# Optimization experiments

Measured on AMD Instinct MI355X. Metric: run time of the kernel, lower is better.

The kernel has to match this reference:

```python
import jax, jax.numpy as jnp
import numpy as np

N_NODES = 100000
EPS = 1e-5


def _layernorm(x, g, b):
    # per-node layer norm over feature dim
    mu = jnp.mean(x, axis=-1, keepdims=True)
    var = jnp.mean(jnp.square(x - mu), axis=-1, keepdims=True)
    return (x - mu) * jax.lax.rsqrt(var + EPS) * g + b


def _gcn_conv(x, W, b, src, dst, n_nodes):
    # GCNConv: xW, then symmetric-normalized aggregation with self-loops.
    xw = x @ W  # [N, out]
    ones = jnp.ones(src.shape[0], dtype=x.dtype)
    deg = jax.ops.segment_sum(ones, dst, num_segments=n_nodes) + 1.0  # +1 self loop
    dinv = jax.lax.rsqrt(deg)  # [N]
    norm = dinv[src] * dinv[dst]  # [E]
    msg = xw[src] * norm[:, None]  # [E, out]  <- dominant memory traffic
    agg = jax.ops.segment_sum(msg, dst, num_segments=n_nodes)
    agg = agg + xw * (dinv * dinv)[:, None]  # self-loop contribution
    return agg + b


def setup_inputs() -> dict:
    key = jax.random.key(0)
    ks = jax.random.split(key, 16)
    in_c, hid, out_c = 128, 64, 32
    E = 1_600_000
    d = {}
    d['x'] = jax.random.normal(ks[0], (N_NODES, in_c), dtype=jnp.float32)
    d['edge_index'] = jax.random.randint(ks[1], (2, E), 0, N_NODES, dtype=jnp.int64)

    def lin(k, fi, fo):
        s = 1.0 / np.sqrt(fi)
        k1, k2 = jax.random.split(k)
        return (jax.random.uniform(k1, (fi, fo), jnp.float32, -s, s),
                jax.random.uniform(k2, (fo,), jnp.float32, -s, s))

    d['W1'], d['b1'] = lin(ks[2], in_c, hid)
    d['g1'], d['be1'] = jnp.ones((hid,), jnp.float32), jnp.zeros((hid,), jnp.float32)
    d['W2'], d['b2'] = lin(ks[3], hid, 2 * hid)
    d['g2'], d['be2'] = jnp.ones((2 * hid,), jnp.float32), jnp.zeros((2 * hid,), jnp.float32)
    d['W3'], d['b3'] = lin(ks[4], 2 * hid, hid)
    d['g3'], d['be3'] = jnp.ones((hid,), jnp.float32), jnp.zeros((hid,), jnp.float32)
    d['lw1'], d['lb1'] = lin(ks[5], hid, hid // 2)
    d['g4'], d['be4'] = jnp.ones((hid // 2,), jnp.float32), jnp.zeros((hid // 2,), jnp.float32)
    d['lw2'], d['lb2'] = lin(ks[6], hid // 2, out_c)
    return d


def reference(x, edge_index, W1, b1, g1, be1, W2, b2, g2, be2, W3, b3, g3, be3,
              lw1, lb1, g4, be4, lw2, lb2):
    src, dst = edge_index[0], edge_index[1]
    h = _gcn_conv(x, W1, b1, src, dst, N_NODES)
    h = jax.nn.elu(_layernorm(h, g1, be1))
    h = _gcn_conv(h, W2, b2, src, dst, N_NODES)
    h = jax.nn.elu(_layernorm(h, g2, be2))
    h = _gcn_conv(h, W3, b3, src, dst, N_NODES)
    h = jax.nn.elu(_layernorm(h, g3, be3))
    h = h @ lw1 + lb1
    h = jax.nn.elu(_layernorm(h, g4, be4))
    return h @ lw2 + lb2
```

## Files before the change

kernel.cpp:

```cpp
#include <hip/hip_runtime.h>
#include <math.h>

#define N_NODES 100000
#define LN_EPS 1e-5f
#define NBUCK ((N_NODES + 255) / 256)
#define EPB 8192

typedef __attribute__((ext_vector_type(8))) short bf16x8;
typedef __attribute__((ext_vector_type(4))) float f32x4;

__device__ __forceinline__ unsigned short f2bf(float f) {
    unsigned int u = __float_as_uint(f);
    return (unsigned short)((u + 0x7FFFu + ((u >> 16) & 1u)) >> 16);
}
__device__ __forceinline__ float bf2f(unsigned short u) {
    return __uint_as_float(((unsigned int)u) << 16);
}


__global__ void count_edges(const int* __restrict__ dst, int* __restrict__ counts, int E) {
    __shared__ int hist[NBUCK];
    for (int b = threadIdx.x; b < NBUCK; b += 512) hist[b] = 0;
    __syncthreads();
    int e0 = blockIdx.x * EPB;
#pragma unroll 4
    for (int i = 0; i < EPB / 512; ++i) {
        int e = e0 + i * 512 + (int)threadIdx.x;
        if (e < E) atomicAdd(&hist[((unsigned)dst[e]) >> 8], 1);
    }
    __syncthreads();
    for (int b = threadIdx.x; b < NBUCK; b += 512)
        counts[blockIdx.x * NBUCK + b] = hist[b];
}

__global__ void scan_pos(const int* __restrict__ counts, int* __restrict__ pos,
                         int* __restrict__ tot, int nblk) {
    __shared__ int s[512];
    int b = blockIdx.x, i = threadIdx.x;
    int v = (i < nblk) ? counts[i * NBUCK + b] : 0;
    s[i] = v;
    __syncthreads();
    for (int off = 1; off < 512; off <<= 1) {
        int t = (i >= off) ? s[i - off] : 0;
        __syncthreads();
        s[i] += t;
        __syncthreads();
    }
    if (i < nblk) pos[i * NBUCK + b] = s[i] - v;
    if (i == 511) tot[b] = s[511];
}

__global__ void scan_base(const int* __restrict__ tot, int* __restrict__ base, int E) {
    __shared__ int s[512];
    int i = threadIdx.x;
    int v = (i < NBUCK) ? tot[i] : 0;
    s[i] = v;
    __syncthreads();
    for (int off = 1; off < 512; off <<= 1) {
        int t = (i >= off) ? s[i - off] : 0;
        __syncthreads();
        s[i] += t;
        __syncthreads();
    }
    if (i < NBUCK) base[i] = s[i] - v;
    if (i == 0) base[NBUCK] = E;
}

__global__ void place_edges(const int* __restrict__ src, const int* __restrict__ dst,
                            const int* __restrict__ pos, const int* __restrict__ base,
                            unsigned* __restrict__ bucket, int E) {
    __shared__ int lcur[NBUCK];
    for (int b = threadIdx.x; b < NBUCK; b += 512)
        lcur[b] = pos[blockIdx.x * NBUCK + b] + base[b];
    __syncthreads();
    int e0 = blockIdx.x * EPB;
#pragma unroll 4
    for (int i = 0; i < EPB / 512; ++i) {
        int e = e0 + i * 512 + (int)threadIdx.x;
        if (e < E) {
            unsigned d = (unsigned)dst[e];
            unsigned s = (unsigned)src[e];
            int p = atomicAdd(&lcur[d >> 8], 1);
            bucket[p] = ((d & 255u) << 24) | s;
        }
    }
}

__global__ void build_csr_node(const unsigned* __restrict__ bucket, const int* __restrict__ base,
                               int* __restrict__ offsets, float* __restrict__ dinv,
                               int* __restrict__ csr, int E) {
    __shared__ int hist[256];
    __shared__ int cur[256];
    int b = blockIdx.x, t = threadIdx.x;
    int r0 = b << 8;
    hist[t] = 0;
    __syncthreads();
    int s0 = base[b], s1 = base[b + 1];
    for (int e = s0 + t; e < s1; e += 256)
        atomicAdd(&hist[bucket[e] >> 24], 1);
    __syncthreads();
    int deg = hist[t];
    for (int off = 1; off < 256; off <<= 1) {
        int tv = (t >= off) ? hist[t - off] : 0;
        __syncthreads();
        hist[t] += tv;
        __syncthreads();
    }
    int excl = hist[t] - deg;
    int node = r0 + t;
    if (node < N_NODES) {
        offsets[node] = s0 + excl;
        dinv[node] = rsqrtf((float)deg + 1.f);
        cur[t] = s0 + excl;
    }
    if (node == N_NODES - 1) offsets[N_NODES] = E;
    __syncthreads();
    for (int e = s0 + t; e < s1; e += 256) {
        unsigned u = bucket[e];
        int p = atomicAdd(&cur[u >> 24], 1);
        csr[p] = (int)(u & 0xFFFFFFu);
    }
}

template <int K, int OUT, bool LN, bool BIAS, bool AF32, bool OF32, bool SCALED>
__launch_bounds__(256)
__global__ void mfma_gemm(const void* __restrict__ Xv, const float* __restrict__ W,
                          const float* __restrict__ bias, const float* __restrict__ gamma,
                          const float* __restrict__ beta, void* __restrict__ Yv, int n,
                          const float* __restrict__ dinvp) {
    constexpr int T  = OUT / 16;
    constexpr int KP = K + 8;

    __shared__ __align__(16) unsigned short sWT[OUT * KP];
    for (int i = threadIdx.x; i < K * OUT; i += 256) {
        int k = i / OUT, o = i - k * OUT;
        sWT[o * KP + k] = f2bf(W[i]);
    }
    __syncthreads();

    int wv = threadIdx.x >> 6, lane = threadIdx.x & 63;
    int quad = lane >> 4, l16 = lane & 15;
    int m0 = (blockIdx.x * 4 + wv) * 16;
    int rowc = min(m0 + l16, n - 1);

    f32x4 acc[T];
#pragma unroll
    for (int t = 0; t < T; ++t) acc[t] = (f32x4){0.f, 0.f, 0.f, 0.f};

#pragma unroll
    for (int s = 0; s < K / 32; ++s) {
        int koff = s * 32 + quad * 8;
        bf16x8 af;
        if (AF32) {
            const float4* X4 = (const float4*)Xv;
            size_t base = ((size_t)rowc * K + koff) >> 2;
            float4 a0 = X4[base];
            float4 a1 = X4[base + 1];
            af[0] = (short)f2bf(a0.x); af[1] = (short)f2bf(a0.y);
            af[2] = (short)f2bf(a0.z); af[3] = (short)f2bf(a0.w);
            af[4] = (short)f2bf(a1.x); af[5] = (short)f2bf(a1.y);
            af[6] = (short)f2bf(a1.z); af[7] = (short)f2bf(a1.w);
        } else {
            const unsigned short* Xb = (const unsigned short*)Xv;
            af = *(const bf16x8*)(Xb + (size_t)rowc * K + koff);
        }
#pragma unroll
        for (int t = 0; t < T; ++t) {
            const bf16x8 bfrag = *(const bf16x8*)&sWT[(t * 16 + l16) * KP + koff];
            acc[t] = __builtin_amdgcn_mfma_f32_16x16x32_bf16(af, bfrag, acc[t], 0, 0, 0);
        }
    }

    float bj[T], gj[T], btj[T];
#pragma unroll
    for (int t = 0; t < T; ++t) {
        int c = t * 16 + l16;
        bj[t]  = BIAS ? bias[c] : 0.f;
        gj[t]  = LN ? gamma[c] : 1.f;
        btj[t] = LN ? beta[c] : 0.f;
    }

    float* Yf = (float*)Yv;
    unsigned short* Yb = (unsigned short*)Yv;

    if (LN) {
        float s[4] = {0.f, 0.f, 0.f, 0.f}, sq[4] = {0.f, 0.f, 0.f, 0.f};
#pragma unroll
        for (int t = 0; t < T; ++t)
#pragma unroll
            for (int r = 0; r < 4; ++r) {
                float v = acc[t][r] + bj[t];
                s[r] += v;
                sq[r] += v * v;
            }
#pragma unroll
        for (int off = 1; off < 16; off <<= 1)
#pragma unroll
            for (int r = 0; r < 4; ++r) {
                s[r] += __shfl_xor(s[r], off, 64);
                sq[r] += __shfl_xor(sq[r], off, 64);
            }
        float mu[4], rs[4];
#pragma unroll
        for (int r = 0; r < 4; ++r) {
            mu[r] = s[r] / OUT;
            float var = sq[r] / OUT - mu[r] * mu[r];
            rs[r] = rsqrtf(var + LN_EPS);
        }
#pragma unroll
        for (int r = 0; r < 4; ++r) {
            int rowg = m0 + quad * 4 + r;
            if (rowg < n) {
                float dv = SCALED ? dinvp[rowg] : 1.f;
#pragma unroll
                for (int t = 0; t < T; ++t) {
                    float y = (acc[t][r] + bj[t] - mu[r]) * rs[r] * gj[t] + btj[t];
                    y = y > 0.f ? y : expm1f(y);
                    if (SCALED) y *= dv;
                    size_t idx = (size_t)rowg * OUT + t * 16 + l16;
                    if (OF32) Yf[idx] = y; else Yb[idx] = f2bf(y);
                }
            }
        }
    } else {
#pragma unroll
        for (int r = 0; r < 4; ++r) {
            int rowg = m0 + quad * 4 + r;
            if (rowg < n) {
                float dv = SCALED ? dinvp[rowg] : 1.f;
#pragma unroll
                for (int t = 0; t < T; ++t) {
                    float y = acc[t][r] + bj[t];
                    if (SCALED) y *= dv;
                    size_t idx = (size_t)rowg * OUT + t * 16 + l16;
                    if (OF32) Yf[idx] = y; else Yb[idx] = f2bf(y);
                }
            }
        }
    }
}

template <bool LN, bool SCALEOUT>
__launch_bounds__(256)
__global__ void gather_d(const unsigned short* __restrict__ xs, const int* __restrict__ offsets,
                         const int* __restrict__ csr_src, const float* __restrict__ dinv,
                         const float* __restrict__ bias, const float* __restrict__ gamma,
                         const float* __restrict__ beta, unsigned short* __restrict__ out, int n) {
    int wave = threadIdx.x >> 6;
    int lane = threadIdx.x & 63;
    int node = blockIdx.x * (blockDim.x >> 6) + wave;
    if (node >= n) return;
    int beg = __builtin_amdgcn_readfirstlane(offsets[node]);
    int end = __builtin_amdgcn_readfirstlane(offsets[node + 1]);

    float a0 = 0.f, a1 = 0.f, a2 = 0.f, a3 = 0.f;
    for (int base = beg; base < end; base += 64) {
        int m = min(64, end - base);
        int myS = (lane < m) ? csr_src[base + lane] : 0;
        for (int k = 0; k < m; k += 16) {
            unsigned short v[16];
            float w[16];
#pragma unroll
            for (int j = 0; j < 16; ++j) {
                int e = k + j;
                int idx = (e < m) ? e : 0;
                int s = __builtin_amdgcn_readlane(myS, idx);
                v[j] = xs[((size_t)(unsigned)s << 6) + lane];
                w[j] = (e < m) ? 1.f : 0.f;
            }
#pragma unroll
            for (int j = 0; j < 16; ++j) {
                float f = bf2f(v[j]) * w[j];
                if ((j & 3) == 0) a0 += f;
                else if ((j & 3) == 1) a1 += f;
                else if ((j & 3) == 2) a2 += f;
                else a3 += f;
            }
        }
    }

    float dd = dinv[node];
    float self = bf2f(xs[((size_t)(unsigned)node << 6) + lane]);
    float y = (a0 + a1 + a2 + a3 + self) * dd;

    if (!LN) {
        out[((size_t)(unsigned)node << 6) + lane] = f2bf(y);
        return;
    }
    float yb = y + bias[lane];
    float s = yb, sq = yb * yb;
#pragma unroll
    for (int off = 1; off < 64; off <<= 1) {
        s += __shfl_xor(s, off, 64);
        sq += __shfl_xor(sq, off, 64);
    }
    float mu = s * (1.f / 64.f);
    float var = sq * (1.f / 64.f) - mu * mu;
    float rs = rsqrtf(var + LN_EPS);
    float z = (yb - mu) * rs * gamma[lane] + beta[lane];
    z = z > 0.f ? z : expm1f(z);
    if (SCALEOUT) z *= dd;
    out[((size_t)(unsigned)node << 6) + lane] = f2bf(z);
}

extern "C" void kernel_launch(void* const* d_in, const int* in_sizes, int n_in,
                              void* d_out, int out_size, void* d_ws, size_t ws_size,
                              hipStream_t stream) {
    const float* x  = (const float*)d_in[0];
    const int* ei   = (const int*)d_in[1];
    const float* W1 = (const float*)d_in[2];
    const float* b1 = (const float*)d_in[3];
    const float* g1 = (const float*)d_in[4];
    const float* be1= (const float*)d_in[5];
    const float* W2 = (const float*)d_in[6];
    const float* b2 = (const float*)d_in[7];
    const float* g2 = (const float*)d_in[8];
    const float* be2= (const float*)d_in[9];
    const float* W3 = (const float*)d_in[10];
    const float* b3 = (const float*)d_in[11];
    const float* g3 = (const float*)d_in[12];
    const float* be3= (const float*)d_in[13];
    const float* lw1= (const float*)d_in[14];
    const float* lb1= (const float*)d_in[15];
    const float* g4 = (const float*)d_in[16];
    const float* be4= (const float*)d_in[17];
    const float* lw2= (const float*)d_in[18];
    const float* lb2= (const float*)d_in[19];
    float* out = (float*)d_out;

    const int E = in_sizes[1] / 2;
    const int* src = ei;
    const int* dst = ei + E;
    const int N = N_NODES;

    unsigned short* bufA = (unsigned short*)d_ws;
    unsigned short* bufB = bufA + (size_t)N * 128;
    float* dinv    = (float*)(bufB + (size_t)N * 128);
    int*   offsets = (int*)(dinv + N);
    int*   csr     = offsets + N + 1;
    int*   tot     = csr + E;
    int*   base    = tot + NBUCK;

    auto cdiv = [](long long a, long long b) { return (int)((a + b - 1) / b); };
    const int NBLK = cdiv(E, EPB);

    int* counts = (int*)bufA;
    int* pos    = counts + (size_t)NBLK * NBUCK;
    unsigned* bucket = (unsigned*)bufB;

    const int GB = cdiv(N, 64);

    count_edges<<<NBLK, 512, 0, stream>>>(dst, counts, E);
    scan_pos<<<NBUCK, 512, 0, stream>>>(counts, pos, tot, NBLK);
    scan_base<<<1, 512, 0, stream>>>(tot, base, E);
    place_edges<<<NBLK, 512, 0, stream>>>(src, dst, pos, base, bucket, E);
    build_csr_node<<<NBUCK, 256, 0, stream>>>(bucket, base, offsets, dinv, csr, E);

    mfma_gemm<128, 64, false, false, true, false, true><<<GB, 256, 0, stream>>>(
        x, W1, nullptr, nullptr, nullptr, bufA, N, dinv);
    gather_d<true, true><<<cdiv(N, 4), 256, 0, stream>>>(bufA, offsets, csr, dinv, b1, g1, be1, bufB, N);

    gather_d<false, false><<<cdiv(N, 4), 256, 0, stream>>>(bufB, offsets, csr, dinv, nullptr, nullptr, nullptr, bufA, N);
    mfma_gemm<64, 128, true, true, false, false, false><<<GB, 256, 0, stream>>>(
        bufA, W2, b2, g2, be2, bufB, N, nullptr);

    mfma_gemm<128, 64, false, false, false, false, true><<<GB, 256, 0, stream>>>(
        bufB, W3, nullptr, nullptr, nullptr, bufA, N, dinv);
    gather_d<true, false><<<cdiv(N, 4), 256, 0, stream>>>(bufA, offsets, csr, dinv, b3, g3, be3, bufB, N);

    mfma_gemm<64, 32, true, true, false, false, false><<<GB, 256, 0, stream>>>(
        bufB, lw1, lb1, g4, be4, bufA, N, nullptr);

    mfma_gemm<32, 32, false, true, false, true, false><<<GB, 256, 0, stream>>>(
        bufA, lw2, lb2, nullptr, nullptr, out, N, nullptr);
}
```

Baseline: 361.9 us.

## Fuse final two linear layers with layernorm and widen gather batching

Adds a lin_fused kernel that runs the 64→32 linear, layernorm, ELU and the 32→32 linear in one pass, keeping the intermediate tile in shared memory instead of writing it to global and launching a second GEMM. The gather kernel now issues up to 32 neighbour loads per batch instead of 16, predicates out-of-range edges rather than loading a dummy row and multiplying by zero, and hoists the self, dinv and LN parameter loads ahead of the loop. The wider batch increases memory-level parallelism at the cost of more registers per thread, which may reduce occupancy.

```diff
diff --git a/kernel.cpp b/kernel.cpp
--- a/kernel.cpp
+++ b/kernel.cpp
@@ -240,6 +240,102 @@
     }
 }
 
+__launch_bounds__(256)
+__global__ void lin_fused(const unsigned short* __restrict__ X, const float* __restrict__ W1f,
+                          const float* __restrict__ b1f, const float* __restrict__ g,
+                          const float* __restrict__ be, const float* __restrict__ W2f,
+                          const float* __restrict__ b2f, float* __restrict__ out, int n) {
+    constexpr int KP1 = 64 + 8;
+    constexpr int KP2 = 32 + 8;
+    constexpr int TS  = 56;
+    __shared__ __align__(16) unsigned short sWT1[32 * KP1];
+    __shared__ __align__(16) unsigned short sWT2[32 * KP2];
+    __shared__ __align__(16) unsigned short sT[4][16 * TS];
+
+    for (int i = threadIdx.x; i < 64 * 32; i += 256) {
+        int k = i >> 5, o = i & 31;
+        sWT1[o * KP1 + k] = f2bf(W1f[i]);
+    }
+    for (int i = threadIdx.x; i < 32 * 32; i += 256) {
+        int k = i >> 5, o = i & 31;
+        sWT2[o * KP2 + k] = f2bf(W2f[i]);
+    }
+    __syncthreads();
+
+    int wv = threadIdx.x >> 6, lane = threadIdx.x & 63;
+    int quad = lane >> 4, l16 = lane & 15;
+    int m0 = (blockIdx.x * 4 + wv) * 16;
+    int rowc = min(m0 + l16, n - 1);
+
+    f32x4 acc[2];
+    acc[0] = (f32x4){0.f, 0.f, 0.f, 0.f};
+    acc[1] = (f32x4){0.f, 0.f, 0.f, 0.f};
+#pragma unroll
+    for (int s = 0; s < 2; ++s) {
+        int koff = s * 32 + quad * 8;
+        bf16x8 af = *(const bf16x8*)(X + (size_t)rowc * 64 + koff);
+#pragma unroll
+        for (int t = 0; t < 2; ++t) {
+            const bf16x8 bfrag = *(const bf16x8*)&sWT1[(t * 16 + l16) * KP1 + koff];
+            acc[t] = __builtin_amdgcn_mfma_f32_16x16x32_bf16(af, bfrag, acc[t], 0, 0, 0);
+        }
+    }
+
+    float bj[2], gj[2], btj[2];
+#pragma unroll
+    for (int t = 0; t < 2; ++t) {
+        int c = t * 16 + l16;
+        bj[t] = b1f[c]; gj[t] = g[c]; btj[t] = be[c];
+    }
+    float s4[4] = {0.f, 0.f, 0.f, 0.f}, sq4[4] = {0.f, 0.f, 0.f, 0.f};
+#pragma unroll
+    for (int t = 0; t < 2; ++t)
+#pragma unroll
+        for (int r = 0; r < 4; ++r) {
+            float v = acc[t][r] + bj[t];
+            s4[r] += v;
+            sq4[r] += v * v;
+        }
+#pragma unroll
+    for (int off = 1; off < 16; off <<= 1)
+#pragma unroll
+        for (int r = 0; r < 4; ++r) {
+            s4[r] += __shfl_xor(s4[r], off, 64);
+            sq4[r] += __shfl_xor(sq4[r], off, 64);
+        }
+#pragma unroll
+    for (int r = 0; r < 4; ++r) {
+        float mu = s4[r] * (1.f / 32.f);
+        float var = sq4[r] * (1.f / 32.f) - mu * mu;
+        float rs = rsqrtf(var + LN_EPS);
+#pragma unroll
+        for (int t = 0; t < 2; ++t) {
+            float z = (acc[t][r] + bj[t] - mu) * rs * gj[t] + btj[t];
+            z = z > 0.f ? z : expm1f(z);
+            sT[wv][(quad * 4 + r) * TS + t * 16 + l16] = f2bf(z);
+        }
+    }
+    __syncthreads();
+
+    bf16x8 a2 = *(const bf16x8*)&sT[wv][l16 * TS + quad * 8];
+    f32x4 acc2[2];
+#pragma unroll
+    for (int t = 0; t < 2; ++t) {
+        const bf16x8 bfrag = *(const bf16x8*)&sWT2[(t * 16 + l16) * KP2 + quad * 8];
+        acc2[t] = __builtin_amdgcn_mfma_f32_16x16x32_bf16(
+            a2, bfrag, (f32x4){0.f, 0.f, 0.f, 0.f}, 0, 0, 0);
+    }
+#pragma unroll
+    for (int r = 0; r < 4; ++r) {
+        int rowg = m0 + quad * 4 + r;
+        if (rowg < n) {
+#pragma unroll
+            for (int t = 0; t < 2; ++t)
+                out[(size_t)rowg * 32 + t * 16 + l16] = acc2[t][r] + b2f[t * 16 + l16];
+        }
+    }
+}
+
 template <bool LN, bool SCALEOUT>
 __launch_bounds__(256)
 __global__ void gather_d(const unsigned short* __restrict__ xs, const int* __restrict__ offsets,
@@ -253,41 +349,47 @@
     int beg = __builtin_amdgcn_readfirstlane(offsets[node]);
     int end = __builtin_amdgcn_readfirstlane(offsets[node + 1]);
 
+    float dd = dinv[node];
+    unsigned short selfv = xs[((unsigned)node << 6) + lane];
+    float bl = LN ? bias[lane] : 0.f;
+    float gl = LN ? gamma[lane] : 1.f;
+    float tl = LN ? beta[lane] : 0.f;
+
     float a0 = 0.f, a1 = 0.f, a2 = 0.f, a3 = 0.f;
     for (int base = beg; base < end; base += 64) {
         int m = min(64, end - base);
         int myS = (lane < m) ? csr_src[base + lane] : 0;
-        for (int k = 0; k < m; k += 16) {
-            unsigned short v[16];
-            float w[16];
-#pragma unroll
-            for (int j = 0; j < 16; ++j) {
-                int e = k + j;
-                int idx = (e < m) ? e : 0;
-                int s = __builtin_amdgcn_readlane(myS, idx);
-                v[j] = xs[((size_t)(unsigned)s << 6) + lane];
-                w[j] = (e < m) ? 1.f : 0.f;
-            }
-#pragma unroll
-            for (int j = 0; j < 16; ++j) {
-                float f = bf2f(v[j]) * w[j];
-                if ((j & 3) == 0) a0 += f;
-                else if ((j & 3) == 1) a1 += f;
-                else if ((j & 3) == 2) a2 += f;
-                else a3 += f;
-            }
-        }
-    }
-
-    float dd = dinv[node];
-    float self = bf2f(xs[((size_t)(unsigned)node << 6) + lane]);
-    float y = (a0 + a1 + a2 + a3 + self) * dd;
+        for (int half = 0; half < m; half += 32) {
+            unsigned short v[32];
+#pragma unroll
+            for (int j = 0; j < 32; ++j) {
+                int e = half + j;
+                if (e < m) {
+                    int s = __builtin_amdgcn_readlane(myS, e);
+                    v[j] = xs[((unsigned)s << 6) + lane];
+                }
+            }
+#pragma unroll
+            for (int j = 0; j < 32; ++j) {
+                int e = half + j;
+                if (e < m) {
+                    float f = bf2f(v[j]);
+                    if ((j & 3) == 0) a0 += f;
+                    else if ((j & 3) == 1) a1 += f;
+                    else if ((j & 3) == 2) a2 += f;
+                    else a3 += f;
+                }
+            }
+        }
+    }
+
+    float y = (a0 + a1 + a2 + a3 + bf2f(selfv)) * dd;
 
     if (!LN) {
-        out[((size_t)(unsigned)node << 6) + lane] = f2bf(y);
+        out[((unsigned)node << 6) + lane] = f2bf(y);
         return;
     }
-    float yb = y + bias[lane];
+    float yb = y + bl;
     float s = yb, sq = yb * yb;
 #pragma unroll
     for (int off = 1; off < 64; off <<= 1) {
@@ -297,10 +399,10 @@
     float mu = s * (1.f / 64.f);
     float var = sq * (1.f / 64.f) - mu * mu;
     float rs = rsqrtf(var + LN_EPS);
-    float z = (yb - mu) * rs * gamma[lane] + beta[lane];
+    float z = (yb - mu) * rs * gl + tl;
     z = z > 0.f ? z : expm1f(z);
     if (SCALEOUT) z *= dd;
-    out[((size_t)(unsigned)node << 6) + lane] = f2bf(z);
+    out[((unsigned)node << 6) + lane] = f2bf(z);
 }
 
 extern "C" void kernel_launch(void* const* d_in, const int* in_sizes, int n_in,
@@ -368,9 +470,5 @@
         bufB, W3, nullptr, nullptr, nullptr, bufA, N, dinv);
     gather_d<true, false><<<cdiv(N, 4), 256, 0, stream>>>(bufA, offsets, csr, dinv, b3, g3, be3, bufB, N);
 
-    mfma_gemm<64, 32, true, true, false, false, false><<<GB, 256, 0, stream>>>(
-        bufB, lw1, lb1, g4, be4, bufA, N, nullptr);
-
-    mfma_gemm<32, 32, false, true, false, true, false><<<GB, 256, 0, stream>>>(
-        bufA, lw2, lb2, nullptr, nullptr, out, N, nullptr);
-}
+    lin_fused<<<GB, 256, 0, stream>>>(bufB, lw1, lb1, g4, be4, lw2, lb2, out, N);
+}
```

New measurement: 545.7 us. +50.8%, slower.
